# Performance work log

Hardware: AMD Instinct MI355X
Metric: run time of the kernel (lower is better)

Reference implementation:

```python
import jax, jax.numpy as jnp
import numpy as np

B, T, IN, H, L, C = 64, 2048, 256, 512, 2, 128


def _uniform(key, shape, bound):
    return jax.random.uniform(key, shape, jnp.float32, -bound, bound)


def setup_inputs() -> dict:
    key = jax.random.key(0)
    ks = jax.random.split(key, 12)
    s = 1.0 / np.sqrt(H)  # PyTorch RNN/Linear init bound
    inp = {
        "x": jax.random.normal(ks[0], (B, T, IN), jnp.float32),
        # layer 0 (input_size -> hidden)
        "W_ih0": _uniform(ks[1], (H, IN), s),
        "W_hh0": _uniform(ks[2], (H, H), s),
        "b_ih0": _uniform(ks[3], (H,), s),
        "b_hh0": _uniform(ks[4], (H,), s),
        # layer 1 (hidden -> hidden)
        "W_ih1": _uniform(ks[5], (H, H), s),
        "W_hh1": _uniform(ks[6], (H, H), s),
        "b_ih1": _uniform(ks[7], (H,), s),
        "b_hh1": _uniform(ks[8], (H,), s),
        # final linear head
        "fc_w": _uniform(ks[9], (C, H), s),
        "fc_b": _uniform(ks[10], (C,), s),
    }
    return inp


def _rnn_layer(x_seq, W_ih, W_hh, b_ih, b_hh):
    """Vanilla ReLU RNN layer: h_t = relu(x_t W_ih^T + b_ih + h_{t-1} W_hh^T + b_hh).
    x_seq: [B, T, D] -> [B, T, H]. Input projection is done as one big GEMM;
    only the recurrent matmul stays inside the scan."""
    pre = jnp.einsum('btd,hd->bth', x_seq, W_ih) + b_ih + b_hh  # [B,T,H]
    h0 = jnp.zeros((x_seq.shape[0], W_hh.shape[0]), x_seq.dtype)

    def step(h, p_t):
        h = jax.nn.relu(p_t + h @ W_hh.T)
        return h, h

    _, hs = jax.lax.scan(step, h0, jnp.swapaxes(pre, 0, 1))  # [T,B,H]
    return jnp.swapaxes(hs, 0, 1)


def reference(x, W_ih0, W_hh0, b_ih0, b_hh0, W_ih1, W_hh1, b_ih1, b_hh1, fc_w, fc_b):
    h = _rnn_layer(x, W_ih0, W_hh0, b_ih0, b_hh0)
    # dropout (rate=0.2) is identity in eval mode -- deterministic reference
    h = _rnn_layer(h, W_ih1, W_hh1, b_ih1, b_hh1)
    last = h[:, -1, :]                 # [B, H]
    return last @ fc_w.T + fc_b        # [B, C]
```

## Files before the change

kernel.cpp:

```cpp
#include <hip/hip_runtime.h>


typedef unsigned short u16;
typedef unsigned int u32;
typedef unsigned long long u64;
typedef _Float16 f16;
typedef _Float16 half8 __attribute__((ext_vector_type(8)));
typedef float float4v __attribute__((ext_vector_type(4)));

#define T_LEN 2048
#define H_DIM 512
#define B_SZ 64
#define SGN 0x8000800080008000ull
#define VMASK 0x7fff7fff7fff7fffull
#define ZMASK 0x0001000100010001ull
#define SPIN_LIM (1 << 15)
#define LAG 7

__device__ __forceinline__ float bf2f(u16 u) {
    union { u32 i; float f; } v; v.i = ((u32)u) << 16; return v.f;
}
__device__ __forceinline__ u16 f2bf(float f) {
    u32 x = __float_as_uint(f);
    u32 r = (x + 0x7fffu + ((x >> 16) & 1u)) >> 16;
    return (u16)r;
}
__device__ __forceinline__ float loadf(const void* p, size_t i, int dt) {
    return dt ? ((const float*)p)[i] : bf2f(((const u16*)p)[i]);
}
__device__ __forceinline__ half8 cvt8_bf16(uint4 v) {
    half8 h;
    h[0] = (f16)bf2f((u16)(v.x & 0xffff)); h[1] = (f16)bf2f((u16)(v.x >> 16));
    h[2] = (f16)bf2f((u16)(v.y & 0xffff)); h[3] = (f16)bf2f((u16)(v.y >> 16));
    h[4] = (f16)bf2f((u16)(v.z & 0xffff)); h[5] = (f16)bf2f((u16)(v.z >> 16));
    h[6] = (f16)bf2f((u16)(v.w & 0xffff)); h[7] = (f16)bf2f((u16)(v.w >> 16));
    return h;
}
__device__ __forceinline__ u64 tagmask(int t) {
    return ((t & 1) ? 0x0000000000008000ull : 0ull) |
           ((t & 2) ? 0x0000000080000000ull : 0ull) |
           ((t & 4) ? 0x0000800000000000ull : 0ull) |
           ((t & 8) ? 0x8000000000000000ull : 0ull);
}
__device__ __forceinline__ u64 ztag(int t) {
    return ((u64)(t & 1)) | ((u64)((t >> 1) & 1) << 16) |
           ((u64)((t >> 2) & 1) << 32) | ((u64)((t >> 3) & 1) << 48);
}
__device__ __forceinline__ u64 aload(u64* p) {
    return __hip_atomic_load(p, __ATOMIC_RELAXED, __HIP_MEMORY_SCOPE_AGENT);
}
__device__ __forceinline__ void astore(u64* p, u64 v) {
    __hip_atomic_store(p, v, __ATOMIC_RELAXED, __HIP_MEMORY_SCOPE_AGENT);
}
__device__ __forceinline__ u32 aload32(u32* p) {
    return __hip_atomic_load(p, __ATOMIC_RELAXED, __HIP_MEMORY_SCOPE_AGENT);
}
__device__ __forceinline__ void astore32(u32* p, u32 v) {
    __hip_atomic_store(p, v, __ATOMIC_RELAXED, __HIP_MEMORY_SCOPE_AGENT);
}
__device__ __forceinline__ float f16u(u16 b) {
    union { u16 u; f16 h; } c; c.u = b; return (float)c.h;
}
__device__ __forceinline__ void scat_store(f16* sbuf, int word, u64 v) {
    int col = word >> 2, q = word & 3;
#pragma unroll
    for (int i = 0; i < 4; ++i) {
        int row = q * 4 + i;
        union { u16 u; f16 h; } c;
        c.u = (u16)(v >> (16 * i));
        sbuf[row * 512 + ((col >> 3) ^ (row & 7)) * 8 + (col & 7)] = c.h;
    }
}

__global__ void detect_kernel(const u16* __restrict__ xr, int* __restrict__ dtf,
                              u32* __restrict__ progP, u32* __restrict__ progL) {
    int lane = threadIdx.x;
    u16 u0 = xr[(lane * 2 + 0) * 2];
    u16 u1 = xr[(lane * 2 + 1) * 2];
    int e0 = (u0 >> 7) & 0xff, e1 = (u1 >> 7) & 0xff;
    int c0 = (e0 >= 0x60 && e0 <= 0x8f) ? 1 : 0;
    int c1 = (e1 >= 0x60 && e1 <= 0x8f) ? 1 : 0;
    int tot = __popcll(__ballot(c0)) + __popcll(__ballot(c1));
    if (lane == 0) *dtf = (tot >= 96) ? 0 : 1;
    progP[lane] = 0;
    progL[lane] = 0;
}

__global__ void cvt_w_kernel(const void* __restrict__ in, f16* __restrict__ out,
                             int n, const int* __restrict__ dtf) {
    int dt = *dtf;
    for (int i = blockIdx.x * blockDim.x + threadIdx.x; i < n; i += gridDim.x * blockDim.x)
        out[i] = (f16)loadf(in, i, dt);
}

__global__ void bias_kernel(const void* __restrict__ bi, const void* __restrict__ bh,
                            float* __restrict__ bias, const int* __restrict__ dtf) {
    int dt = *dtf;
    int i = blockIdx.x * blockDim.x + threadIdx.x;
    if (i < H_DIM) bias[i] = loadf(bi, i, dt) + loadf(bh, i, dt);
}

__global__ void fcb_kernel(const void* __restrict__ in, float* __restrict__ out,
                           const int* __restrict__ dtf) {
    int i = threadIdx.x;
    if (i < 128) out[i] = loadf(in, i, *dtf);
}

__global__ void initz_kernel(u64* __restrict__ hexZ) {
    int i = blockIdx.x * blockDim.x + threadIdx.x;
    hexZ[i] = 0x0001000100010001ull;
}

template<int RAW>
__global__ __launch_bounds__(256)
void gemm_tiled(const void* __restrict__ Araw, const f16* __restrict__ Bw,
                const float* __restrict__ bias, f16* __restrict__ C,
                int lgTc, int t_off, int K, const int* __restrict__ dtf)
{
    __shared__ f16 As[64][40];
    __shared__ f16 Bs[64][40];
    const int dt = RAW ? *dtf : 0;
    const int m0 = blockIdx.x * 64, n0 = blockIdx.y * 64;
    const int tid = threadIdx.x;
    const int wv = tid >> 6, lane = tid & 63;
    const int lr = lane & 15, quad = lane >> 4;
    const int srow = tid >> 2, skq = tid & 3;

    float4v acc[4] = {{0.f,0.f,0.f,0.f},{0.f,0.f,0.f,0.f},{0.f,0.f,0.f,0.f},{0.f,0.f,0.f,0.f}};

    size_t arow;
    {
        int ml = m0 + srow;
        if (RAW) {
            int b = ml >> lgTc, tt = ml & ((1 << lgTc) - 1);
            arow = (size_t)b * T_LEN + t_off + tt;
        } else arow = (size_t)ml;
    }
    const f16* pb = Bw + (size_t)(n0 + srow) * K + skq * 8;

    for (int k0 = 0; k0 < K; k0 += 32) {
        half8 av;
        if (RAW) {
            if (dt) {
                const float* ap = (const float*)Araw + arow * K + k0 + skq * 8;
                float4v f0 = *(const float4v*)ap;
                float4v f1 = *(const float4v*)(ap + 4);
                av[0]=(f16)f0[0]; av[1]=(f16)f0[1]; av[2]=(f16)f0[2]; av[3]=(f16)f0[3];
                av[4]=(f16)f1[0]; av[5]=(f16)f1[1]; av[6]=(f16)f1[2]; av[7]=(f16)f1[3];
            } else {
                av = cvt8_bf16(*(const uint4*)((const u16*)Araw + arow * K + k0 + skq * 8));
            }
        } else {
            av = *(const half8*)((const f16*)Araw + arow * K + k0 + skq * 8);
        }
        half8 bv = *(const half8*)(pb + k0);
        __syncthreads();
        *(half8*)&As[srow][skq * 8] = av;
        *(half8*)&Bs[srow][skq * 8] = bv;
        __syncthreads();
        half8 bf = *(const half8*)&Bs[wv * 16 + lr][quad * 8];
#pragma unroll
        for (int mt = 0; mt < 4; ++mt) {
            half8 af = *(const half8*)&As[mt * 16 + lr][quad * 8];
            acc[mt] = __builtin_amdgcn_mfma_f32_16x16x32_f16(af, bf, acc[mt], 0, 0, 0);
        }
    }
    const int n = n0 + wv * 16 + lr;
    const float bval = bias[n];
#pragma unroll
    for (int mt = 0; mt < 4; ++mt) {
#pragma unroll
        for (int i = 0; i < 4; ++i) {
            int m = m0 + mt * 16 + quad * 4 + i;
            C[(size_t)m * H_DIM + n] = (f16)(acc[mt][i] + bval);
        }
    }
}

__global__ __launch_bounds__(256, 1)
void rnn_scan3(const f16* __restrict__ pre0,
               const f16* __restrict__ Whh0,
               const f16* __restrict__ Wih1,
               const f16* __restrict__ Whh1,
               const float* __restrict__ bias1,
               u64* __restrict__ hex0,
               u64* __restrict__ hex1,
               u64* __restrict__ hexZ,
               f16* __restrict__ hc0,
               f16* __restrict__ hc1,
               u32* __restrict__ progP,
               u32* __restrict__ progL,
               int t0, int Tc,
               float* __restrict__ h_last)
{
    __shared__ f16 stage[2][16 * 512];
    __shared__ f16 sH0[16 * 512];
    const int b = blockIdx.x;
    int role, r, cg;
    if (b < 32) { int c = b & 7; role = c >> 2; r = c & 3; cg = b >> 3; }
    else        { role = 2; r = (b - 32) >> 2; cg = (b - 32) & 3; }
    const int rows0 = r * 16;
    const int tid = threadIdx.x;
    const int w = tid >> 6, lane = tid & 63;
    const int lr = lane & 15, quad = lane >> 4;
    const int c0w = cg * 128 + w * 32;
    const int wbase = tid * 8;
    const bool mine = (tid >> 6) == cg;

    if (role == 2) {
        half8 Bp[2][16];
#pragma unroll
        for (int j = 0; j < 2; ++j)
#pragma unroll
            for (int kc = 0; kc < 16; ++kc)
                Bp[j][kc] = *(const half8*)(Wih1 + (size_t)(c0w + j * 16 + lr) * H_DIM
                                            + kc * 32 + quad * 8);
        float bvv[2] = { bias1[c0w + lr], bias1[c0w + 16 + lr] };
        const int z0 = (c0w + lr) * 4 + quad;

        u64 vv[8];
        {
            u64* src = hex0 + ((size_t)(t0 & 7) * 4 + r) * 2048;
#pragma unroll
            for (int k = 0; k < 8; ++k) vv[k] = aload(&src[wbase + k]);
        }

        for (int tt = 0; tt < Tc; ++tt) {
            const int t = t0 + tt;
            const int nb = t & 7;
            const u64 em = tagmask(t);
            const int need = t - LAG;
            const u32 want = (u32)(need + 1);

            u32 plv = 0xffffffffu;
            if (need >= 0) plv = aload32(&progL[r]);

            {
                u64* src = hex0 + ((size_t)nb * 4 + r) * 2048;
                int pend = 0;
#pragma unroll
                for (int k = 0; k < 8; ++k)
                    if ((vv[k] & SGN) != em) pend |= 1 << k;
                int guard = 0;
                while (pend && guard < SPIN_LIM) {
#pragma unroll
                    for (int k = 0; k < 8; ++k)
                        if (pend & (1 << k)) vv[k] = aload(&src[wbase + k]);
#pragma unroll
                    for (int k = 0; k < 8; ++k)
                        if ((pend & (1 << k)) && ((vv[k] & SGN) == em))
                            pend &= ~(1 << k);
                    ++guard;
                }
#pragma unroll
                for (int k = 0; k < 8; ++k)
                    scat_store(sH0, wbase + k, vv[k] & VMASK);
            }
            __syncthreads();
            if (tid == 0) astore32(&progP[r * 4 + cg], (u32)(t + 1));

            float4v acc0 = {0.f,0.f,0.f,0.f}, acc1 = {0.f,0.f,0.f,0.f};
#pragma unroll
            for (int kc = 0; kc < 16; ++kc) {
                half8 a = *(const half8*)&sH0[lr * 512 + (((kc * 4 + quad) ^ (lr & 7)) * 8)];
                acc0 = __builtin_amdgcn_mfma_f32_16x16x32_f16(a, Bp[0][kc], acc0, 0, 0, 0);
                acc1 = __builtin_amdgcn_mfma_f32_16x16x32_f16(a, Bp[1][kc], acc1, 0, 0, 0);
            }

            const u64 ez = ztag(t);
            u64 zw[2];
#pragma unroll
            for (int j = 0; j < 2; ++j) {
                const float4v& a = j ? acc1 : acc0;
                u64 wp = 0;
#pragma unroll
                for (int i = 0; i < 4; ++i) {
                    union { f16 h; u16 u; } c;
                    c.h = (f16)(a[i] + bvv[j]);
                    wp |= ((u64)(c.u & 0xFFFEu)) << (16 * i);
                }
                zw[j] = wp | ez;
            }

            if (need >= 0) {
                int g = 0;
                while (plv < want && g < SPIN_LIM) { plv = aload32(&progL[r]); ++g; }
            }
            {
                u64* dz = hexZ + ((size_t)nb * 4 + r) * 2048;
                astore(&dz[z0], zw[0]);
                astore(&dz[z0 + 64], zw[1]);
            }
            if (tt + 1 < Tc) {
                u64* srcn = hex0 + ((size_t)((t + 1) & 7) * 4 + r) * 2048;
#pragma unroll
                for (int k = 0; k < 8; ++k) vv[k] = aload(&srcn[wbase + k]);
            }
            __syncthreads();
        }
        return;
    }

    const f16* Wrec = role ? Whh1 : Whh0;
    f16* hcar = role ? hc1 : hc0;
    u64* hexOwn = role ? hex1 : hex0;

    half8 Bf[2][16];
#pragma unroll
    for (int j = 0; j < 2; ++j)
#pragma unroll
        for (int kc = 0; kc < 16; ++kc)
            Bf[j][kc] = *(const half8*)(Wrec + (size_t)(c0w + j * 16 + lr) * H_DIM
                                        + kc * 32 + quad * 8);

    if (t0 > 0) {
        int row = tid >> 4, g0 = (tid & 15) * 4;
#pragma unroll
        for (int gq = 0; gq < 4; ++gq) {
            int g = g0 + gq;
            *(uint4*)&stage[(t0 - 1) & 1][row * 512 + ((g ^ (row & 7)) * 8)] =
                *(const uint4*)(hcar + (size_t)(rows0 + row) * H_DIM + g * 8);
        }
    }
    __syncthreads();

    u64 sv[8];
    u64 vvz[2];
    const int z0 = (c0w + lr) * 4 + quad;
    if (role) {
        u64* zb = hexZ + ((size_t)(t0 & 7) * 4 + r) * 2048;
        vvz[0] = aload(&zb[z0]);
        vvz[1] = aload(&zb[z0 + 64]);
    }
    f16 pvh[2][4];
    if (!role) {
#pragma unroll
        for (int j = 0; j < 2; ++j)
#pragma unroll
            for (int i = 0; i < 4; ++i)
                pvh[j][i] = pre0[((size_t)(rows0 + quad * 4 + i) * Tc + 0) * H_DIM
                                 + c0w + j * 16 + lr];
    }

    for (int tt = 0; tt < Tc; ++tt) {
        const int t = t0 + tt;
        const int p = (t - 1) & 1, np = t & 1;
        const u64 em = tagmask(t);
        const int nbOwn = role ? (t & 1) : (t & 7);
        const int need = t - LAG;
        const u32 want = (u32)(need + 1);

        u32 ppv = 0xffffffffu;
        if (!role && need >= 0 && lane < 4)
            ppv = aload32(&progP[r * 4 + lane]);

        if (tt > 0 && !mine) {
            u64* src = hexOwn + ((size_t)(role ? ((t - 1) & 1) : ((t - 1) & 7)) * 4 + r) * 2048;
            const u64 emp = tagmask(t - 1);
            int pend = 0;
#pragma unroll
            for (int k = 0; k < 8; ++k)
                if ((sv[k] & SGN) != emp) pend |= 1 << k;
            int guard = 0;
            while (pend && guard < SPIN_LIM) {
#pragma unroll
                for (int k = 0; k < 8; ++k)
                    if (pend & (1 << k)) sv[k] = aload(&src[wbase + k]);
#pragma unroll
                for (int k = 0; k < 8; ++k)
                    if ((pend & (1 << k)) && ((sv[k] & SGN) == emp))
                        pend &= ~(1 << k);
                ++guard;
            }
#pragma unroll
            for (int k = 0; k < 8; ++k)
                scat_store(stage[p], wbase + k, sv[k] & VMASK);
        }
        __syncthreads();

        if (role && tid == 0) astore32(&progL[r], (u32)t);

        float4v acc0 = {0.f,0.f,0.f,0.f}, acc1 = {0.f,0.f,0.f,0.f};
        if (t > 0) {
            const f16* sb = stage[p];
#pragma unroll
            for (int kc = 0; kc < 16; ++kc) {
                half8 a = *(const half8*)&sb[lr * 512 + (((kc * 4 + quad) ^ (lr & 7)) * 8)];
                acc0 = __builtin_amdgcn_mfma_f32_16x16x32_f16(a, Bf[0][kc], acc0, 0, 0, 0);
                acc1 = __builtin_amdgcn_mfma_f32_16x16x32_f16(a, Bf[1][kc], acc1, 0, 0, 0);
            }
        }

        if (role) {
            u64* zb = hexZ + ((size_t)(t & 7) * 4 + r) * 2048;
            const u64 ez = ztag(t);
            int pend = 0;
            if ((vvz[0] & ZMASK) != ez) pend |= 1;
            if ((vvz[1] & ZMASK) != ez) pend |= 2;
            int guard = 0;
            while (pend && guard < SPIN_LIM) {
                if (pend & 1) { vvz[0] = aload(&zb[z0]);      if ((vvz[0] & ZMASK) == ez) pend &= ~1; }
                if (pend & 2) { vvz[1] = aload(&zb[z0 + 64]); if ((vvz[1] & ZMASK) == ez) pend &= ~2; }
                ++guard;
            }
        }

        f16 hv[2][4];
        u64 pw[2];
#pragma unroll
        for (int j = 0; j < 2; ++j) {
            const float4v& a = j ? acc1 : acc0;
            u64 wp = 0;
#pragma unroll
            for (int i = 0; i < 4; ++i) {
                float pvv;
                if (role) pvv = f16u((u16)((vvz[j] >> (16 * i)) & 0xFFFEu));
                else      pvv = (float)pvh[j][i];
                float hval = fmaxf(a[i] + pvv, 0.f);
                hv[j][i] = (f16)hval;
                union { f16 h; u16 u; } c; c.h = hv[j][i];
                wp |= ((u64)c.u) << (16 * i);
            }
            pw[j] = wp | em;
        }
        if (!role && need >= 0) {
            bool ok = __all((lane < 4) ? (ppv >= want) : 1);
            int g = 0;
            while (!ok && g < SPIN_LIM) {
                if (lane < 4) ppv = aload32(&progP[r * 4 + lane]);
                ok = __all((lane < 4) ? (ppv >= want) : 1);
                ++g;
            }
        }
        {
            u64* dst = hexOwn + ((size_t)nbOwn * 4 + r) * 2048;
            astore(&dst[z0], pw[0]);
            astore(&dst[z0 + 64], pw[1]);
        }
#pragma unroll
        for (int j = 0; j < 2; ++j)
#pragma unroll
            for (int i = 0; i < 4; ++i) {
                int row = quad * 4 + i, lc = c0w + j * 16 + lr;
                stage[np][row * 512 + ((lc >> 3) ^ (row & 7)) * 8 + (lc & 7)] = hv[j][i];
            }
        if (role && h_last && t == T_LEN - 1) {
#pragma unroll
            for (int j = 0; j < 2; ++j)
#pragma unroll
                for (int i = 0; i < 4; ++i)
                    h_last[(size_t)(rows0 + quad * 4 + i) * H_DIM + c0w + j * 16 + lr] =
                        (float)hv[j][i];
        }
        if (tt == Tc - 1) {
#pragma unroll
            for (int j = 0; j < 2; ++j)
#pragma unroll
                for (int i = 0; i < 4; ++i)
                    hcar[(size_t)(rows0 + quad * 4 + i) * H_DIM + c0w + j * 16 + lr] =
                        hv[j][i];
        }
        if (!mine) {
            u64* src = hexOwn + ((size_t)nbOwn * 4 + r) * 2048;
#pragma unroll
            for (int k = 0; k < 8; ++k) sv[k] = aload(&src[wbase + k]);
        }
        if (tt + 1 < Tc) {
            if (!role) {
#pragma unroll
                for (int j = 0; j < 2; ++j)
#pragma unroll
                    for (int i = 0; i < 4; ++i)
                        pvh[j][i] = pre0[((size_t)(rows0 + quad * 4 + i) * Tc + tt + 1)
                                         * H_DIM + c0w + j * 16 + lr];
            } else {
                u64* zb = hexZ + ((size_t)((t + 1) & 7) * 4 + r) * 2048;
                vvz[0] = aload(&zb[z0]);
                vvz[1] = aload(&zb[z0 + 64]);
            }
        }
    }
}

__global__ void fc_kernel(const float* __restrict__ hlast, const f16* __restrict__ fcw,
                          const float* __restrict__ fcb, void* __restrict__ out,
                          const int* __restrict__ dtf) {
    int b = blockIdx.x, c = threadIdx.x;
    const float* hrow = hlast + b * H_DIM;
    const f16* wrow = fcw + (size_t)c * H_DIM;
    float s = fcb[c];
    for (int h0 = 0; h0 < H_DIM; h0 += 8) {
        half8 w = *(const half8*)(wrow + h0);
#pragma unroll
        for (int j = 0; j < 8; ++j) s += hrow[h0 + j] * (float)w[j];
    }
    if (*dtf) ((float*)out)[b * 128 + c] = s;
    else      ((u16*)out)[b * 128 + c] = f2bf(s);
}

extern "C" void kernel_launch(void* const* d_in, const int* in_sizes, int n_in,
                              void* d_out, int out_size, void* d_ws, size_t ws_size,
                              hipStream_t stream)
{
    const void* x     = d_in[0];
    const void* W_ih0 = d_in[1];
    const void* W_hh0 = d_in[2];
    const void* b_ih0 = d_in[3];
    const void* b_hh0 = d_in[4];
    const void* W_ih1 = d_in[5];
    const void* W_hh1 = d_in[6];
    const void* b_ih1 = d_in[7];
    const void* b_hh1 = d_in[8];
    const void* fc_w  = d_in[9];
    const void* fc_b  = d_in[10];

    char* ws = (char*)d_ws;
    int*   dtf   = (int*)(ws + 0);
    float* bias0 = (float*)(ws + 4096);
    float* bias1 = (float*)(ws + 6144);
    float* fcbf  = (float*)(ws + 8192);
    u32*   progP = (u32*)(ws + 12288);
    u32*   progL = (u32*)(ws + 12544);
    float* hlast = (float*)(ws + 16384);
    f16*   hc0   = (f16*)(ws + 147456);
    f16*   hc1   = (f16*)(ws + 212992);
    u64*   hex0  = (u64*)(ws + 278528);
    u64*   hex1  = (u64*)(ws + 802816);
    u64*   hexZ  = (u64*)(ws + 933888);
    f16*   Wih0f = (f16*)(ws + 1458176);
    f16*   Whh0f = (f16*)(ws + 1720320);
    f16*   Wih1f = (f16*)(ws + 2244608);
    f16*   Whh1f = (f16*)(ws + 2768896);
    f16*   fcwf  = (f16*)(ws + 3293184);

    const size_t misc = 4u << 20;
    int Tc = 128;
    {
        auto need = [&](int tc) {
            return misc + (size_t)B_SZ * (size_t)tc * H_DIM * 2;
        };
        if (ws_size >= need(2048)) Tc = 2048;
        else if (ws_size >= need(1024)) Tc = 1024;
        else if (ws_size >= need(512)) Tc = 512;
        else if (ws_size >= need(256)) Tc = 256;
        else Tc = 128;
    }
    int lgTc = 31 - __builtin_clz((unsigned)Tc);
    f16* bufA = (f16*)(ws + misc);

    detect_kernel<<<dim3(1), dim3(64), 0, stream>>>((const u16*)x, dtf, progP, progL);
    initz_kernel<<<dim3(256), dim3(256), 0, stream>>>(hexZ);
    cvt_w_kernel<<<dim3(512), dim3(256), 0, stream>>>(W_ih0, Wih0f, H_DIM * 256, dtf);
    cvt_w_kernel<<<dim3(1024), dim3(256), 0, stream>>>(W_hh0, Whh0f, H_DIM * H_DIM, dtf);
    cvt_w_kernel<<<dim3(1024), dim3(256), 0, stream>>>(W_ih1, Wih1f, H_DIM * H_DIM, dtf);
    cvt_w_kernel<<<dim3(1024), dim3(256), 0, stream>>>(W_hh1, Whh1f, H_DIM * H_DIM, dtf);
    cvt_w_kernel<<<dim3(256), dim3(256), 0, stream>>>(fc_w, fcwf, 128 * H_DIM, dtf);
    bias_kernel<<<dim3(2), dim3(256), 0, stream>>>(b_ih0, b_hh0, bias0, dtf);
    bias_kernel<<<dim3(2), dim3(256), 0, stream>>>(b_ih1, b_hh1, bias1, dtf);
    fcb_kernel<<<dim3(1), dim3(128), 0, stream>>>(fc_b, fcbf, dtf);

    const int NC = T_LEN / Tc;
    const int mblocks = B_SZ * Tc / 64;
    for (int c = 0; c < NC; ++c) {
        const int t0 = c * Tc;
        gemm_tiled<1><<<dim3(mblocks, 8), 256, 0, stream>>>(
            x, Wih0f, bias0, bufA, lgTc, t0, 256, dtf);
        rnn_scan3<<<dim3(48), dim3(256), 0, stream>>>(
            bufA, Whh0f, Wih1f, Whh1f, bias1, hex0, hex1, hexZ, hc0, hc1,
            progP, progL, t0, Tc, hlast);
    }
    fc_kernel<<<dim3(B_SZ), dim3(128), 0, stream>>>(hlast, fcwf, fcbf, d_out, dtf);
}
```

Before: 6.371 ms.

## Split each recurrent row-group across two blocks with LDS-resident weights and split K

Recurrent blocks drop from four column-group blocks per row group to two, each owning 256 output columns. Half of each block's W_hh slice stays in registers and the other half is cached in a 128x512 LDS buffer. The K-reduction is split so the half of h computed locally is multiplied before the block waits for the peer's half, overlapping the exchange with MFMA work. Fewer blocks means less cross-block exchange traffic, but each block does twice the MFMA work per step and the progL gating becomes per-half, adding LDS pressure and more synchronisation complexity.

```diff
diff --git a/kernel.cpp b/kernel.cpp
--- a/kernel.cpp
+++ b/kernel.cpp
@@ -193,30 +193,29 @@
                int t0, int Tc,
                float* __restrict__ h_last)
 {
-    __shared__ f16 stage[2][16 * 512];
-    __shared__ f16 sH0[16 * 512];
+    __shared__ f16 stage[16 * 512];
+    __shared__ f16 big[128 * 512];
     const int b = blockIdx.x;
-    int role, r, cg;
-    if (b < 32) { int c = b & 7; role = c >> 2; r = c & 3; cg = b >> 3; }
-    else        { role = 2; r = (b - 32) >> 2; cg = (b - 32) & 3; }
-    const int rows0 = r * 16;
     const int tid = threadIdx.x;
     const int w = tid >> 6, lane = tid & 63;
     const int lr = lane & 15, quad = lane >> 4;
-    const int c0w = cg * 128 + w * 32;
-    const int wbase = tid * 8;
-    const bool mine = (tid >> 6) == cg;
-
-    if (role == 2) {
+
+    if (b >= 16) {
+        const int pr = b - 16;
+        const int r = pr >> 2, q = pr & 3;
+        f16* sH0 = big;
+        const int c0p = q * 128 + w * 32;
         half8 Bp[2][16];
 #pragma unroll
         for (int j = 0; j < 2; ++j)
 #pragma unroll
             for (int kc = 0; kc < 16; ++kc)
-                Bp[j][kc] = *(const half8*)(Wih1 + (size_t)(c0w + j * 16 + lr) * H_DIM
+                Bp[j][kc] = *(const half8*)(Wih1 + (size_t)(c0p + j * 16 + lr) * H_DIM
                                             + kc * 32 + quad * 8);
-        float bvv[2] = { bias1[c0w + lr], bias1[c0w + 16 + lr] };
-        const int z0 = (c0w + lr) * 4 + quad;
+        float bvv[2] = { bias1[c0p + lr], bias1[c0p + 16 + lr] };
+        const int z0 = (c0p + lr) * 4 + quad;
+        const int wbase = tid * 8;
+        const int sgate = r * 2 + (q >> 1);
 
         u64 vv[8];
         {
@@ -233,7 +232,7 @@
             const u32 want = (u32)(need + 1);
 
             u32 plv = 0xffffffffu;
-            if (need >= 0) plv = aload32(&progL[r]);
+            if (need >= 0) plv = aload32(&progL[sgate]);
 
             {
                 u64* src = hex0 + ((size_t)nb * 4 + r) * 2048;
@@ -257,7 +256,7 @@
                     scat_store(sH0, wbase + k, vv[k] & VMASK);
             }
             __syncthreads();
-            if (tid == 0) astore32(&progP[r * 4 + cg], (u32)(t + 1));
+            if (tid == 0) astore32(&progP[r * 4 + q], (u32)(t + 1));
 
             float4v acc0 = {0.f,0.f,0.f,0.f}, acc1 = {0.f,0.f,0.f,0.f};
 #pragma unroll
@@ -284,7 +283,7 @@
 
             if (need >= 0) {
                 int g = 0;
-                while (plv < want && g < SPIN_LIM) { plv = aload32(&progL[r]); ++g; }
+                while (plv < want && g < SPIN_LIM) { plv = aload32(&progL[sgate]); ++g; }
             }
             {
                 u64* dz = hexZ + ((size_t)nb * 4 + r) * 2048;
@@ -301,9 +300,16 @@
         return;
     }
 
+    const int s = b >> 3;
+    const int c = b & 7;
+    const int role = c >> 2;
+    const int r = c & 3;
+    const int rows0 = r * 16;
+    const int c0w = s * 256 + w * 64;
     const f16* Wrec = role ? Whh1 : Whh0;
     f16* hcar = role ? hc1 : hc0;
     u64* hexOwn = role ? hex1 : hex0;
+    f16* WL = big;
 
     half8 Bf[2][16];
 #pragma unroll
@@ -313,113 +319,140 @@
             Bf[j][kc] = *(const half8*)(Wrec + (size_t)(c0w + j * 16 + lr) * H_DIM
                                         + kc * 32 + quad * 8);
 
+    {
+        for (int it = 0; it < 32; ++it) {
+            int idx = tid * 32 + it;
+            int cl = idx >> 6, g = idx & 63;
+            int gc = s * 256 + (cl >> 5) * 64 + 32 + (cl & 31);
+            *(uint4*)&WL[cl * 512 + ((g ^ (cl & 7)) * 8)] =
+                *(const uint4*)(Wrec + (size_t)gc * H_DIM + g * 8);
+        }
+    }
+
     if (t0 > 0) {
         int row = tid >> 4, g0 = (tid & 15) * 4;
 #pragma unroll
         for (int gq = 0; gq < 4; ++gq) {
             int g = g0 + gq;
-            *(uint4*)&stage[(t0 - 1) & 1][row * 512 + ((g ^ (row & 7)) * 8)] =
+            *(uint4*)&stage[row * 512 + ((g ^ (row & 7)) * 8)] =
                 *(const uint4*)(hcar + (size_t)(rows0 + row) * H_DIM + g * 8);
         }
     }
-    __syncthreads();
-
-    u64 sv[8];
-    u64 vvz[2];
+
+    const int cl2 = w * 32 + lr, cl3 = cl2 + 16;
     const int z0 = (c0w + lr) * 4 + quad;
+    const int wr0 = (1 - s) * 1024 + tid * 4;
+
+    u64 sv[4];
+    u64 vvz[4];
     if (role) {
         u64* zb = hexZ + ((size_t)(t0 & 7) * 4 + r) * 2048;
-        vvz[0] = aload(&zb[z0]);
-        vvz[1] = aload(&zb[z0 + 64]);
-    }
-    f16 pvh[2][4];
+#pragma unroll
+        for (int k = 0; k < 4; ++k) vvz[k] = aload(&zb[z0 + k * 64]);
+    }
+    f16 pvh[4][4];
     if (!role) {
 #pragma unroll
-        for (int j = 0; j < 2; ++j)
+        for (int j = 0; j < 4; ++j)
 #pragma unroll
             for (int i = 0; i < 4; ++i)
                 pvh[j][i] = pre0[((size_t)(rows0 + quad * 4 + i) * Tc + 0) * H_DIM
                                  + c0w + j * 16 + lr];
     }
 
+#define MF4(KC) do {                                                          \
+    half8 _a = *(const half8*)&stage[lr * 512 +                               \
+                                     ((((KC) * 4 + quad) ^ (lr & 7)) * 8)];   \
+    acc[0] = __builtin_amdgcn_mfma_f32_16x16x32_f16(_a, Bf[0][(KC)], acc[0], 0, 0, 0); \
+    acc[1] = __builtin_amdgcn_mfma_f32_16x16x32_f16(_a, Bf[1][(KC)], acc[1], 0, 0, 0); \
+    half8 _b2 = *(const half8*)&WL[cl2 * 512 + ((((KC) * 4 + quad) ^ (cl2 & 7)) * 8)]; \
+    half8 _b3 = *(const half8*)&WL[cl3 * 512 + ((((KC) * 4 + quad) ^ (cl3 & 7)) * 8)]; \
+    acc[2] = __builtin_amdgcn_mfma_f32_16x16x32_f16(_a, _b2, acc[2], 0, 0, 0); \
+    acc[3] = __builtin_amdgcn_mfma_f32_16x16x32_f16(_a, _b3, acc[3], 0, 0, 0); \
+} while (0)
+#define DP_LO() do { MF4(0); MF4(1); MF4(2); MF4(3); MF4(4); MF4(5); MF4(6); MF4(7); } while (0)
+#define DP_HI() do { MF4(8); MF4(9); MF4(10); MF4(11); MF4(12); MF4(13); MF4(14); MF4(15); } while (0)
+
     for (int tt = 0; tt < Tc; ++tt) {
         const int t = t0 + tt;
-        const int p = (t - 1) & 1, np = t & 1;
         const u64 em = tagmask(t);
         const int nbOwn = role ? (t & 1) : (t & 7);
         const int need = t - LAG;
         const u32 want = (u32)(need + 1);
 
+        __syncthreads();
+
+        if (role && tid == 0) astore32(&progL[r * 2 + s], (u32)t);
+
         u32 ppv = 0xffffffffu;
         if (!role && need >= 0 && lane < 4)
             ppv = aload32(&progP[r * 4 + lane]);
 
-        if (tt > 0 && !mine) {
+        float4v acc[4] = {{0.f,0.f,0.f,0.f},{0.f,0.f,0.f,0.f},
+                          {0.f,0.f,0.f,0.f},{0.f,0.f,0.f,0.f}};
+
+        if (t > 0) { if (s == 0) DP_LO(); else DP_HI(); }
+
+        if (tt > 0) {
             u64* src = hexOwn + ((size_t)(role ? ((t - 1) & 1) : ((t - 1) & 7)) * 4 + r) * 2048;
             const u64 emp = tagmask(t - 1);
             int pend = 0;
 #pragma unroll
-            for (int k = 0; k < 8; ++k)
+            for (int k = 0; k < 4; ++k)
                 if ((sv[k] & SGN) != emp) pend |= 1 << k;
             int guard = 0;
             while (pend && guard < SPIN_LIM) {
 #pragma unroll
-                for (int k = 0; k < 8; ++k)
-                    if (pend & (1 << k)) sv[k] = aload(&src[wbase + k]);
-#pragma unroll
-                for (int k = 0; k < 8; ++k)
+                for (int k = 0; k < 4; ++k)
+                    if (pend & (1 << k)) sv[k] = aload(&src[wr0 + k]);
+#pragma unroll
+                for (int k = 0; k < 4; ++k)
                     if ((pend & (1 << k)) && ((sv[k] & SGN) == emp))
                         pend &= ~(1 << k);
                 ++guard;
             }
 #pragma unroll
-            for (int k = 0; k < 8; ++k)
-                scat_store(stage[p], wbase + k, sv[k] & VMASK);
+            for (int k = 0; k < 4; ++k)
+                scat_store(stage, wr0 + k, sv[k] & VMASK);
         }
         __syncthreads();
 
-        if (role && tid == 0) astore32(&progL[r], (u32)t);
-
-        float4v acc0 = {0.f,0.f,0.f,0.f}, acc1 = {0.f,0.f,0.f,0.f};
-        if (t > 0) {
-            const f16* sb = stage[p];
-#pragma unroll
-            for (int kc = 0; kc < 16; ++kc) {
-                half8 a = *(const half8*)&sb[lr * 512 + (((kc * 4 + quad) ^ (lr & 7)) * 8)];
-                acc0 = __builtin_amdgcn_mfma_f32_16x16x32_f16(a, Bf[0][kc], acc0, 0, 0, 0);
-                acc1 = __builtin_amdgcn_mfma_f32_16x16x32_f16(a, Bf[1][kc], acc1, 0, 0, 0);
-            }
-        }
+        if (t > 0) { if (s == 0) DP_HI(); else DP_LO(); }
 
         if (role) {
             u64* zb = hexZ + ((size_t)(t & 7) * 4 + r) * 2048;
             const u64 ez = ztag(t);
             int pend = 0;
-            if ((vvz[0] & ZMASK) != ez) pend |= 1;
-            if ((vvz[1] & ZMASK) != ez) pend |= 2;
+#pragma unroll
+            for (int k = 0; k < 4; ++k)
+                if ((vvz[k] & ZMASK) != ez) pend |= 1 << k;
             int guard = 0;
             while (pend && guard < SPIN_LIM) {
-                if (pend & 1) { vvz[0] = aload(&zb[z0]);      if ((vvz[0] & ZMASK) == ez) pend &= ~1; }
-                if (pend & 2) { vvz[1] = aload(&zb[z0 + 64]); if ((vvz[1] & ZMASK) == ez) pend &= ~2; }
+#pragma unroll
+                for (int k = 0; k < 4; ++k)
+                    if (pend & (1 << k)) vvz[k] = aload(&zb[z0 + k * 64]);
+#pragma unroll
+                for (int k = 0; k < 4; ++k)
+                    if ((pend & (1 << k)) && ((vvz[k] & ZMASK) == ez))
+                        pend &= ~(1 << k);
                 ++guard;
             }
         }
 
-        f16 hv[2][4];
-        u64 pw[2];
-#pragma unroll
-        for (int j = 0; j < 2; ++j) {
-            const float4v& a = j ? acc1 : acc0;
+        f16 hv[4][4];
+        u64 pw[4];
+#pragma unroll
+        for (int j = 0; j < 4; ++j) {
             u64 wp = 0;
 #pragma unroll
             for (int i = 0; i < 4; ++i) {
                 float pvv;
                 if (role) pvv = f16u((u16)((vvz[j] >> (16 * i)) & 0xFFFEu));
                 else      pvv = (float)pvh[j][i];
-                float hval = fmaxf(a[i] + pvv, 0.f);
+                float hval = fmaxf(acc[j][i] + pvv, 0.f);
                 hv[j][i] = (f16)hval;
-                union { f16 h; u16 u; } c; c.h = hv[j][i];
-                wp |= ((u64)c.u) << (16 * i);
+                union { f16 h; u16 u; } cu2; cu2.h = hv[j][i];
+                wp |= ((u64)cu2.u) << (16 * i);
             }
             pw[j] = wp | em;
         }
@@ -434,19 +467,19 @@
         }
         {
             u64* dst = hexOwn + ((size_t)nbOwn * 4 + r) * 2048;
-            astore(&dst[z0], pw[0]);
-            astore(&dst[z0 + 64], pw[1]);
-        }
-#pragma unroll
-        for (int j = 0; j < 2; ++j)
+#pragma unroll
+            for (int j = 0; j < 4; ++j) astore(&dst[z0 + j * 64], pw[j]);
+        }
+#pragma unroll
+        for (int j = 0; j < 4; ++j)
 #pragma unroll
             for (int i = 0; i < 4; ++i) {
                 int row = quad * 4 + i, lc = c0w + j * 16 + lr;
-                stage[np][row * 512 + ((lc >> 3) ^ (row & 7)) * 8 + (lc & 7)] = hv[j][i];
+                stage[row * 512 + ((lc >> 3) ^ (row & 7)) * 8 + (lc & 7)] = hv[j][i];
             }
         if (role && h_last && t == T_LEN - 1) {
 #pragma unroll
-            for (int j = 0; j < 2; ++j)
+            for (int j = 0; j < 4; ++j)
 #pragma unroll
                 for (int i = 0; i < 4; ++i)
                     h_last[(size_t)(rows0 + quad * 4 + i) * H_DIM + c0w + j * 16 + lr] =
@@ -454,32 +487,35 @@
         }
         if (tt == Tc - 1) {
 #pragma unroll
-            for (int j = 0; j < 2; ++j)
+            for (int j = 0; j < 4; ++j)
 #pragma unroll
                 for (int i = 0; i < 4; ++i)
                     hcar[(size_t)(rows0 + quad * 4 + i) * H_DIM + c0w + j * 16 + lr] =
                         hv[j][i];
         }
-        if (!mine) {
+        {
             u64* src = hexOwn + ((size_t)nbOwn * 4 + r) * 2048;
 #pragma unroll
-            for (int k = 0; k < 8; ++k) sv[k] = aload(&src[wbase + k]);
+            for (int k = 0; k < 4; ++k) sv[k] = aload(&src[wr0 + k]);
         }
         if (tt + 1 < Tc) {
             if (!role) {
 #pragma unroll
-                for (int j = 0; j < 2; ++j)
+                for (int j = 0; j < 4; ++j)
 #pragma unroll
                     for (int i = 0; i < 4; ++i)
                         pvh[j][i] = pre0[((size_t)(rows0 + quad * 4 + i) * Tc + tt + 1)
                                          * H_DIM + c0w + j * 16 + lr];
             } else {
                 u64* zb = hexZ + ((size_t)((t + 1) & 7) * 4 + r) * 2048;
-                vvz[0] = aload(&zb[z0]);
-                vvz[1] = aload(&zb[z0 + 64]);
-            }
-        }
-    }
+#pragma unroll
+                for (int k = 0; k < 4; ++k) vvz[k] = aload(&zb[z0 + k * 64]);
+            }
+        }
+    }
+#undef MF4
+#undef DP_LO
+#undef DP_HI
 }
 
 __global__ void fc_kernel(const float* __restrict__ hlast, const f16* __restrict__ fcw,
@@ -565,7 +601,7 @@
         const int t0 = c * Tc;
         gemm_tiled<1><<<dim3(mblocks, 8), 256, 0, stream>>>(
             x, Wih0f, bias0, bufA, lgTc, t0, 256, dtf);
-        rnn_scan3<<<dim3(48), dim3(256), 0, stream>>>(
+        rnn_scan3<<<dim3(32), dim3(256), 0, stream>>>(
             bufA, Whh0f, Wih1f, Whh1f, bias1, hex0, hex1, hexZ, hc0, hc1,
             progP, progL, t0, Tc, hlast);
     }
```

After: 6.684 ms. 1.05x slower.
